# Performance work log

Measured on AMD Instinct MI355X. Metric: run time of the kernel, lower is better.

Reference implementation:

```python
import jax, jax.numpy as jnp
import numpy as np

D_MODEL = 768
N_HEADS = 12
D_K = 768
D_V = 768
SEQ = 2048
BATCH = 2


def setup_inputs() -> dict:
    key = jax.random.key(0)
    ks = jax.random.split(key, 9)
    s = 0.02
    return {
        "x": jax.random.normal(ks[0], (SEQ, BATCH, D_MODEL), dtype=jnp.float32),
        "Wq": jax.random.normal(ks[1], (D_MODEL, D_K), dtype=jnp.float32) * s,
        "bq": jnp.zeros((D_K,), dtype=jnp.float32),
        "Wk": jax.random.normal(ks[2], (D_MODEL, D_K), dtype=jnp.float32) * s,
        "bk": jnp.zeros((D_K,), dtype=jnp.float32),
        "Wv": jax.random.normal(ks[3], (D_MODEL, D_V), dtype=jnp.float32) * s,
        "bv": jnp.zeros((D_V,), dtype=jnp.float32),
        "Wo": jax.random.normal(ks[4], (D_V, D_MODEL), dtype=jnp.float32) * s,
        "bo": jnp.zeros((D_MODEL,), dtype=jnp.float32),
    }


def reference(x, Wq, bq, Wk, bk, Wv, bv, Wo, bo):
    # x: (S, B, D)
    S, B, D = x.shape
    H = N_HEADS
    hk = D_K // H
    hv = D_V // H
    q = (x @ Wq + bq).reshape(S, B, H, hk)
    k = (x @ Wk + bk).reshape(S, B, H, hk)
    v = (x @ Wv + bv).reshape(S, B, H, hv)
    scale = 1.0 / np.sqrt(hk).astype(np.float32)
    # scores: (B, H, S_q, S_k)
    att = jnp.einsum("sbhd,tbhd->bhst", q, k) * scale
    causal = jnp.triu(jnp.ones((S, S), dtype=bool), k=1)  # True above diagonal
    att = jnp.where(causal, jnp.float32(-jnp.inf), att)
    att = jax.nn.softmax(att, axis=-1)
    y = jnp.einsum("bhst,tbhd->sbhd", att, v).reshape(S, B, D_V)
    return y @ Wo + bo  # (S, B, D)
```

## Files before the change

### kernel.cpp

```cpp
#include <hip/hip_runtime.h>

typedef __attribute__((ext_vector_type(8))) short short8;
typedef __attribute__((ext_vector_type(4))) short s16x4;
typedef __attribute__((ext_vector_type(4))) float f32x4;

#define NHEADS 12
#define SEQLEN 2048
#define HEADD  64
#define DMODEL 768

__device__ __forceinline__ short cvtbf(float f) {
  unsigned u = __builtin_bit_cast(unsigned, f);
  u += 0x7fffu + ((u >> 16) & 1u);
  return (short)(u >> 16);
}

__device__ __forceinline__ void gload16(const void* g, void* l) {
  __builtin_amdgcn_global_load_lds((const __attribute__((address_space(1))) void*)g,
                                   (__attribute__((address_space(3))) void*)l, 16, 0, 0);
}

__device__ __forceinline__ void ds_write_hi16(short* p, float v) {
  asm volatile("ds_write_b16_d16_hi %0, %1"
               : : "v"((__attribute__((address_space(3))) short*)p), "v"(v) : "memory");
}

__global__ void prep_kernel(const float* __restrict__ x, short* __restrict__ xb,
                            const float* __restrict__ w0, const float* __restrict__ w1,
                            const float* __restrict__ w2, const float* __restrict__ w3,
                            short* __restrict__ wt, short* __restrict__ wot) {
  __shared__ float t[32][33];
  const int tid = threadIdx.x;
  if (blockIdx.x < 1536) {
    int i = blockIdx.x * 256 + tid;
    const float* p = x + (size_t)i * 8;
    short8 v;
#pragma unroll
    for (int j = 0; j < 8; ++j) v[j] = cvtbf(p[j]);
    *(short8*)(xb + (size_t)i * 8) = v;
    return;
  }
  int bx = blockIdx.x - 1536;
  int bz = bx / 576, rem = bx - bz * 576;
  int bxx = rem % 24, byy = rem / 24;
  const float* W = bz == 0 ? w0 : bz == 1 ? w1 : bz == 2 ? w2 : w3;
  short* O = bz < 3 ? wt + (size_t)bz * (768 * 768) : wot;
  int tx = tid & 31, ty = tid >> 5;
  int n0 = bxx * 32, k0 = byy * 32;
#pragma unroll
  for (int j = 0; j < 4; ++j)
    t[ty + j * 8][tx] = W[(k0 + ty + j * 8) * 768 + n0 + tx];
  __syncthreads();
#pragma unroll
  for (int j = 0; j < 4; ++j)
    O[(n0 + ty + j * 8) * 768 + k0 + tx] = cvtbf(t[tx][ty + j * 8]);
}

template <bool DBUF>
__device__ __forceinline__ void gemm_core128(const short* __restrict__ A,
                                             const short* __restrict__ Bt,
                                             short* sA, short* sB,
                                             int bm, int bn, f32x4 acc[4][4]) {
  const int tid = threadIdx.x;
  const int w = tid >> 6, lane = tid & 63;
  const int quad = lane >> 4, l16 = lane & 15;
  const int wm = (w & 1) * 64, wn = (w >> 1) * 64;

  int gA[4], gB[4], lbase[4];
#pragma unroll
  for (int j = 0; j < 4; ++j) {
    int slot = j * 256 + w * 64 + lane;
    int r = slot >> 3, c = (slot & 7) ^ (r & 7);
    gA[j] = (bm * 128 + r) * 768 + c * 8;
    gB[j] = (bn * 128 + r) * 768 + c * 8;
    lbase[j] = (j * 256 + w * 64) * 8;
  }

  if (DBUF) {
#pragma unroll
    for (int j = 0; j < 4; ++j) {
      gload16(A + gA[j], sA + lbase[j]);
      gload16(Bt + gB[j], sB + lbase[j]);
    }
    int pb = 0;
    for (int kt = 0; kt < 12; ++kt) {
      __syncthreads();
      if (kt + 1 < 12) {
        int o = (pb ^ 1) * 8192;
#pragma unroll
        for (int j = 0; j < 4; ++j) {
          gload16(A + gA[j] + (kt + 1) * 64, sA + o + lbase[j]);
          gload16(Bt + gB[j] + (kt + 1) * 64, sB + o + lbase[j]);
        }
      }
      const short* pa = sA + pb * 8192;
      const short* pbv = sB + pb * 8192;
#pragma unroll
      for (int ks = 0; ks < 2; ++ks) {
        int cp = (ks * 4 + quad) ^ (l16 & 7);
        short8 a[4], b[4];
#pragma unroll
        for (int mt = 0; mt < 4; ++mt)
          a[mt] = *(const short8*)(pa + (wm + mt * 16 + l16) * 64 + cp * 8);
#pragma unroll
        for (int nt = 0; nt < 4; ++nt)
          b[nt] = *(const short8*)(pbv + (wn + nt * 16 + l16) * 64 + cp * 8);
#pragma unroll
        for (int mt = 0; mt < 4; ++mt)
#pragma unroll
          for (int nt = 0; nt < 4; ++nt)
            acc[mt][nt] = __builtin_amdgcn_mfma_f32_16x16x32_bf16(a[mt], b[nt], acc[mt][nt], 0, 0, 0);
      }
      pb ^= 1;
    }
  } else {
    for (int kt = 0; kt < 12; ++kt) {
      __syncthreads();
#pragma unroll
      for (int j = 0; j < 4; ++j) {
        gload16(A + gA[j] + kt * 64, sA + lbase[j]);
        gload16(Bt + gB[j] + kt * 64, sB + lbase[j]);
      }
      __syncthreads();
#pragma unroll
      for (int ks = 0; ks < 2; ++ks) {
        int cp = (ks * 4 + quad) ^ (l16 & 7);
        short8 a[4], b[4];
#pragma unroll
        for (int mt = 0; mt < 4; ++mt)
          a[mt] = *(const short8*)(sA + (wm + mt * 16 + l16) * 64 + cp * 8);
#pragma unroll
        for (int nt = 0; nt < 4; ++nt)
          b[nt] = *(const short8*)(sB + (wn + nt * 16 + l16) * 64 + cp * 8);
#pragma unroll
        for (int mt = 0; mt < 4; ++mt)
#pragma unroll
          for (int nt = 0; nt < 4; ++nt)
            acc[mt][nt] = __builtin_amdgcn_mfma_f32_16x16x32_bf16(a[mt], b[nt], acc[mt][nt], 0, 0, 0);
      }
    }
  }
}

__global__ __launch_bounds__(256, 3) void qkv_gemm(
    const short* __restrict__ A, const short* __restrict__ Bt,
    const float* __restrict__ bq, const float* __restrict__ bk, const float* __restrict__ bv,
    short* __restrict__ oq, short* __restrict__ ok, short* __restrict__ ov) {
  __shared__ short sA[128 * 64];
  __shared__ short sB[128 * 64];
  f32x4 acc[4][4];
  const f32x4 z4 = {0.f, 0.f, 0.f, 0.f};
#pragma unroll
  for (int mt = 0; mt < 4; ++mt)
#pragma unroll
    for (int nt = 0; nt < 4; ++nt) acc[mt][nt] = z4;

  const int bm = blockIdx.x, bn = blockIdx.y;
  gemm_core128<false>(A, Bt, sA, sB, bm, bn, acc);

  const int seg = bn / 6, bn_l = bn % 6;
  const float* bias = seg == 0 ? bq : seg == 1 ? bk : bv;
  short* outp = seg == 0 ? oq : seg == 1 ? ok : ov;

  const int tid = threadIdx.x;
  const int w = tid >> 6, lane = tid & 63;
  const int quad = lane >> 4, l16 = lane & 15;
  const int wm = (w & 1) * 64, wn = (w >> 1) * 64;

#pragma unroll
  for (int nt = 0; nt < 4; ++nt) {
    int n = bn_l * 128 + wn + nt * 16 + l16;
    float bval = bias[n];
    int h = n >> 6, d = n & 63;
#pragma unroll
    for (int mt = 0; mt < 4; ++mt) {
      int rowb = wm + mt * 16 + quad * 4;
#pragma unroll
      for (int r = 0; r < 4; ++r) {
        int m = bm * 128 + rowb + r;
        int s = m >> 1, b = m & 1;
        float v = acc[mt][nt][r] + bval;
        if (seg == 0) v *= 0.1803368801f;
        if (seg < 2)
          outp[((b * NHEADS + h) * SEQLEN + s) * HEADD + d] = cvtbf(v);
        else
          outp[((b * NHEADS + h) * HEADD + d) * SEQLEN + s] = cvtbf(v);
      }
    }
  }
}

#define AE(qi, ts, nt) ((qi) | ((ts) << 8) | ((nt) << 16))
__device__ const int ATTN_TAB[80] = {
  AE(31,0,8), AE(31,8,8), AE(31,16,8), AE(31,24,8),
  AE(30,0,8), AE(30,8,8), AE(30,16,8),
  AE(29,0,8), AE(29,8,8), AE(29,16,8),
  AE(28,0,8), AE(28,8,8), AE(28,16,8),
  AE(27,0,8), AE(27,8,8), AE(27,16,8),
  AE(26,0,8), AE(26,8,8), AE(26,16,8),
  AE(25,0,8), AE(25,8,8), AE(25,16,8),
  AE(24,0,8), AE(24,8,8), AE(24,16,8),
  AE(23,0,8), AE(23,8,8), AE(23,16,8),
  AE(22,0,8), AE(22,8,8),
  AE(21,0,8), AE(21,8,8),
  AE(20,0,8), AE(20,8,8),
  AE(19,0,8), AE(19,8,8),
  AE(18,0,8), AE(18,8,8),
  AE(17,0,8), AE(17,8,8),
  AE(16,0,8), AE(16,8,8),
  AE(15,0,8), AE(15,8,8),
  AE(14,0,8), AE(13,0,8), AE(12,0,8), AE(11,0,8),
  AE(10,0,8), AE(9,0,8),  AE(8,0,8),  AE(7,0,8),
  AE(30,24,7), AE(22,16,7), AE(14,8,7), AE(6,0,7),
  AE(29,24,6), AE(21,16,6), AE(13,8,6), AE(5,0,6),
  AE(28,24,5), AE(20,16,5), AE(12,8,5), AE(4,0,5),
  AE(27,24,4), AE(19,16,4), AE(11,8,4), AE(3,0,4),
  AE(26,24,3), AE(18,16,3), AE(10,8,3), AE(2,0,3),
  AE(25,24,2), AE(17,16,2), AE(9,8,2),  AE(1,0,2),
  AE(24,24,1), AE(16,16,1), AE(8,8,1),  AE(0,0,1),
};
__device__ const int PBASE[32] = {
  0,0,0,0,0,0,0,0,
  0,2,4,6,8,10,12,14,
  16,19,22,25,28,31,34,37,
  40,44,48,52,56,60,64,68};

__global__ __launch_bounds__(128, 2) void attn_kernel(
    const short* __restrict__ Q, const short* __restrict__ K,
    const short* __restrict__ Vt, short* __restrict__ Y,
    float* __restrict__ Of, float* __restrict__ lf) {
  __shared__ short sK[2][64 * 64];
  __shared__ short sV[2][64 * 64];
  __shared__ short sP[64 * 64];
  const int tid = threadIdx.x;
  const int w = tid >> 6, lane = tid & 63;
  const int quad = lane >> 4, l16 = lane & 15;
  const int e = ATTN_TAB[blockIdx.x / 24];
  const int bh = blockIdx.x % 24;
  const int qi = e & 255, ts = (e >> 8) & 255, ntl = e >> 16;
  const int q0 = qi << 6;
  const short* Qb = Q + (size_t)bh * (SEQLEN * HEADD);
  const short* Kb = K + (size_t)bh * (SEQLEN * HEADD);
  const short* Vb = Vt + (size_t)bh * (SEQLEN * HEADD);

  short8 aq[2][2];
#pragma unroll
  for (int m = 0; m < 2; ++m)
#pragma unroll
    for (int ks = 0; ks < 2; ++ks)
      aq[m][ks] = *(const short8*)(Qb + (q0 + w * 32 + m * 16 + l16) * 64 + ks * 32 + quad * 8);

  const short8 bones = {0x3F80, 0x3F80, 0x3F80, 0x3F80, 0x3F80, 0x3F80, 0x3F80, 0x3F80};
  f32x4 acc_o[2][4], acc_l[2];
  const f32x4 z4 = {0.f, 0.f, 0.f, 0.f};
#pragma unroll
  for (int m = 0; m < 2; ++m) {
#pragma unroll
    for (int nt = 0; nt < 4; ++nt) acc_o[m][nt] = z4;
    acc_l[m] = z4;
  }

  int gK[4], gV[4], lbase[4];
#pragma unroll
  for (int j = 0; j < 4; ++j) {
    int slot = j * 128 + w * 64 + lane;
    int r = slot >> 3, c = (slot & 7) ^ (r & 7);
    gK[j] = r * 64 + c * 8;
    gV[j] = r * 2048 + c * 8;
    lbase[j] = (j * 128 + w * 64) * 8;
  }

  const int tend = ts + ntl;

#pragma unroll
  for (int j = 0; j < 4; ++j) {
    gload16(Kb + (ts << 6) * 64 + gK[j], &sK[0][lbase[j]]);
    gload16(Vb + (ts << 6) + gV[j], &sV[0][lbase[j]]);
  }

  int pb = 0;
  for (int it = ts; it < tend; ++it) {
    __syncthreads();
    if (it + 1 < tend) {
      const int t1 = (it + 1) << 6;
#pragma unroll
      for (int j = 0; j < 4; ++j) {
        gload16(Kb + t1 * 64 + gK[j], &sK[pb ^ 1][lbase[j]]);
        gload16(Vb + t1 + gV[j], &sV[pb ^ 1][lbase[j]]);
      }
    }
    const short* sk = sK[pb];
    const short* sv = sV[pb];

    f32x4 sc[2][4];
#pragma unroll
    for (int m = 0; m < 2; ++m)
#pragma unroll
      for (int nt = 0; nt < 4; ++nt) sc[m][nt] = z4;
    __builtin_amdgcn_s_setprio(1);
#pragma unroll
    for (int ks = 0; ks < 2; ++ks) {
      int cp = (ks * 4 + quad) ^ (l16 & 7);
#pragma unroll
      for (int nt = 0; nt < 4; ++nt) {
        short8 bk = *(const short8*)(sk + (nt * 16 + l16) * 64 + cp * 8);
#pragma unroll
        for (int m = 0; m < 2; ++m)
          sc[m][nt] = __builtin_amdgcn_mfma_f32_16x16x32_bf16(aq[m][ks], bk, sc[m][nt], 0, 0, 0);
      }
    }
    __builtin_amdgcn_s_setprio(0);

    if (it == qi) {
      const int t0 = it << 6;
#pragma unroll
      for (int m = 0; m < 2; ++m) {
        int qrow = q0 + w * 32 + m * 16 + quad * 4;
#pragma unroll
        for (int nt = 0; nt < 4; ++nt)
#pragma unroll
          for (int r = 0; r < 4; ++r) {
            int t = t0 + nt * 16 + l16;
            if (t > qrow + r) sc[m][nt][r] = -1e30f;
          }
      }
    }

#pragma unroll
    for (int m = 0; m < 2; ++m)
#pragma unroll
      for (int nt = 0; nt < 4; ++nt)
#pragma unroll
        for (int r = 0; r < 4; ++r) {
          float p = __builtin_amdgcn_exp2f(sc[m][nt][r]);
          int rq = w * 32 + m * 16 + quad * 4 + r;
          int t = nt * 16 + l16;
          int c = t >> 3;
          ds_write_hi16(&sP[rq * 64 + ((c ^ (rq & 7)) * 8 + (t & 7))], p);
        }

    __builtin_amdgcn_s_setprio(1);
#pragma unroll
    for (int kst = 0; kst < 2; ++kst) {
      short8 ap[2];
#pragma unroll
      for (int m = 0; m < 2; ++m) {
        int rq = w * 32 + m * 16 + l16;
        int cpa = (kst * 4 + quad) ^ (rq & 7);
        ap[m] = *(const short8*)(sP + rq * 64 + cpa * 8);
        acc_l[m] = __builtin_amdgcn_mfma_f32_16x16x32_bf16(ap[m], bones, acc_l[m], 0, 0, 0);
      }
#pragma unroll
      for (int nt = 0; nt < 4; ++nt) {
        int row = nt * 16 + l16;
        int cv = (kst * 4 + quad) ^ (row & 7);
        short8 bv = *(const short8*)(sv + row * 64 + cv * 8);
#pragma unroll
        for (int m = 0; m < 2; ++m)
          acc_o[m][nt] = __builtin_amdgcn_mfma_f32_16x16x32_bf16(ap[m], bv, acc_o[m][nt], 0, 0, 0);
      }
    }
    __builtin_amdgcn_s_setprio(0);
    pb ^= 1;
  }

  if (qi < 8) {
    const int b = bh / NHEADS, h = bh % NHEADS;
#pragma unroll
    for (int m = 0; m < 2; ++m)
#pragma unroll
      for (int r = 0; r < 4; ++r) {
        float rl = __builtin_amdgcn_rcpf(acc_l[m][r]);
        int srow = q0 + w * 32 + m * 16 + quad * 4 + r;
#pragma unroll
        for (int nt = 0; nt < 4; ++nt)
          Y[(srow * 2 + b) * DMODEL + h * 64 + nt * 16 + l16] = cvtbf(acc_o[m][nt][r] * rl);
      }
  } else {
    const int slot = bh * 72 + PBASE[qi] + (ts >> 3);
    float* Ob = Of + (size_t)slot * 4096;
#pragma unroll
    for (int m = 0; m < 2; ++m)
#pragma unroll
      for (int r = 0; r < 4; ++r) {
        int row = w * 32 + m * 16 + quad * 4 + r;
#pragma unroll
        for (int nt = 0; nt < 4; ++nt)
          Ob[row * 64 + nt * 16 + l16] = acc_o[m][nt][r];
        if (l16 == 0) lf[slot * 64 + row] = acc_l[m][r];
      }
  }
}

__global__ void attn_merge(const float* __restrict__ Of, const float* __restrict__ lf,
                           short* __restrict__ Y) {
  const int bh = blockIdx.x % 24, qi = 8 + blockIdx.x / 24;
  const int nch = (qi >> 3) + 1;
  const int base = bh * 72 + PBASE[qi];
  const float* O0 = Of + (size_t)base * 4096;
  const float* L0 = lf + base * 64;
  const int b = bh / NHEADS, h = bh % NHEADS;
  const int tid = threadIdx.x;
#pragma unroll
  for (int j = 0; j < 4; ++j) {
    int i4 = j * 256 + tid;
    int row = i4 >> 4, col4 = (i4 & 15) * 4;
    f32x4 o = *(const f32x4*)(O0 + (size_t)i4 * 4);
    float l = L0[row];
    for (int c = 1; c < nch; ++c) {
      o += *(const f32x4*)(O0 + (size_t)c * 4096 + (size_t)i4 * 4);
      l += L0[c * 64 + row];
    }
    float rl = __builtin_amdgcn_rcpf(l);
    s16x4 y;
#pragma unroll
    for (int k = 0; k < 4; ++k) y[k] = cvtbf(o[k] * rl);
    int srow = qi * 64 + row;
    *(s16x4*)(Y + (size_t)(srow * 2 + b) * DMODEL + h * 64 + col4) = y;
  }
}

__global__ __launch_bounds__(256, 2) void oproj_gemm(
    const short* __restrict__ A, const short* __restrict__ Bt,
    const float* __restrict__ bo, float* __restrict__ out) {
  __shared__ short sA[2 * 128 * 64];
  __shared__ short sB[2 * 128 * 64];
  f32x4 acc[4][4];
  const f32x4 z4 = {0.f, 0.f, 0.f, 0.f};
#pragma unroll
  for (int mt = 0; mt < 4; ++mt)
#pragma unroll
    for (int nt = 0; nt < 4; ++nt) acc[mt][nt] = z4;

  const int bm = blockIdx.x, bn = blockIdx.y;
  gemm_core128<true>(A, Bt, sA, sB, bm, bn, acc);

  const int tid = threadIdx.x;
  const int w = tid >> 6, lane = tid & 63;
  const int quad = lane >> 4, l16 = lane & 15;
  const int wm = (w & 1) * 64, wn = (w >> 1) * 64;

#pragma unroll
  for (int nt = 0; nt < 4; ++nt) {
    int n = bn * 128 + wn + nt * 16 + l16;
    float bval = bo[n];
#pragma unroll
    for (int mt = 0; mt < 4; ++mt) {
      int rowb = wm + mt * 16 + quad * 4;
#pragma unroll
      for (int r = 0; r < 4; ++r) {
        int m = bm * 128 + rowb + r;
        out[(size_t)m * 768 + n] = acc[mt][nt][r] + bval;
      }
    }
  }
}

extern "C" void kernel_launch(void* const* d_in, const int* in_sizes, int n_in,
                              void* d_out, int out_size, void* d_ws, size_t ws_size,
                              hipStream_t stream) {
  const float* x  = (const float*)d_in[0];
  const float* Wq = (const float*)d_in[1];
  const float* bq = (const float*)d_in[2];
  const float* Wk = (const float*)d_in[3];
  const float* bk = (const float*)d_in[4];
  const float* Wv = (const float*)d_in[5];
  const float* bv = (const float*)d_in[6];
  const float* Wo = (const float*)d_in[7];
  const float* bo = (const float*)d_in[8];
  float* out = (float*)d_out;

  short* ws  = (short*)d_ws;
  short* xb  = ws;
  short* wt  = ws + 3145728;
  short* wot = ws + 4915200;
  short* qw  = ws + 5505024;
  short* kw  = ws + 8650752;
  short* vw  = ws + 11796480;
  short* yw  = ws + 14942208;
  float* Of  = (float*)(ws + 18087936);
  float* lf  = Of + 7077888;

  prep_kernel<<<3840, 256, 0, stream>>>(x, xb, Wq, Wk, Wv, Wo, wt, wot);
  qkv_gemm<<<dim3(32, 18), 256, 0, stream>>>(xb, wt, bq, bk, bv, qw, kw, vw);
  attn_kernel<<<1920, 128, 0, stream>>>(qw, kw, vw, yw, Of, lf);
  attn_merge<<<576, 256, 0, stream>>>(Of, lf, yw);
  oproj_gemm<<<dim3(32, 6), 256, 0, stream>>>(yw, wot, bo, out);
}
```

Before: 157.2 us.

## Double attention query tile to 128 rows per block with new split-K schedule

The attention kernel now processes 128 query rows per block with 4 waves (256 threads), so each staged K/V tile is shared by twice as many queries. The work table is rebuilt for 16 query pairs with uneven KV chunk splits, the partial-output buffers and merge kernel are resized to 128-row slots, and the causal mask now applies for any tile at or past the diagonal pair. The s_setprio hints are removed. This cuts the number of blocks and redundant K/V loads, but it raises LDS and register pressure per block and changes load balance.

```diff
diff --git a/kernel.cpp b/kernel.cpp
--- a/kernel.cpp
+++ b/kernel.cpp
@@ -190,55 +190,47 @@
   }
 }
 
-#define AE(qi, ts, nt) ((qi) | ((ts) << 8) | ((nt) << 16))
-__device__ const int ATTN_TAB[80] = {
-  AE(31,0,8), AE(31,8,8), AE(31,16,8), AE(31,24,8),
-  AE(30,0,8), AE(30,8,8), AE(30,16,8),
-  AE(29,0,8), AE(29,8,8), AE(29,16,8),
-  AE(28,0,8), AE(28,8,8), AE(28,16,8),
-  AE(27,0,8), AE(27,8,8), AE(27,16,8),
-  AE(26,0,8), AE(26,8,8), AE(26,16,8),
-  AE(25,0,8), AE(25,8,8), AE(25,16,8),
-  AE(24,0,8), AE(24,8,8), AE(24,16,8),
-  AE(23,0,8), AE(23,8,8), AE(23,16,8),
-  AE(22,0,8), AE(22,8,8),
-  AE(21,0,8), AE(21,8,8),
-  AE(20,0,8), AE(20,8,8),
-  AE(19,0,8), AE(19,8,8),
-  AE(18,0,8), AE(18,8,8),
-  AE(17,0,8), AE(17,8,8),
-  AE(16,0,8), AE(16,8,8),
-  AE(15,0,8), AE(15,8,8),
-  AE(14,0,8), AE(13,0,8), AE(12,0,8), AE(11,0,8),
-  AE(10,0,8), AE(9,0,8),  AE(8,0,8),  AE(7,0,8),
-  AE(30,24,7), AE(22,16,7), AE(14,8,7), AE(6,0,7),
-  AE(29,24,6), AE(21,16,6), AE(13,8,6), AE(5,0,6),
-  AE(28,24,5), AE(20,16,5), AE(12,8,5), AE(4,0,5),
-  AE(27,24,4), AE(19,16,4), AE(11,8,4), AE(3,0,4),
-  AE(26,24,3), AE(18,16,3), AE(10,8,3), AE(2,0,3),
-  AE(25,24,2), AE(17,16,2), AE(9,8,2),  AE(1,0,2),
-  AE(24,24,1), AE(16,16,1), AE(8,8,1),  AE(0,0,1),
+#define AE(qip, ts, nt, ci) ((qip) | ((ts) << 8) | ((nt) << 16) | ((ci) << 24))
+__device__ const int ATTN_TAB[40] = {
+  AE(15,0,8,0), AE(15,8,8,1), AE(15,16,8,2), AE(15,24,8,3),
+  AE(14,0,8,0), AE(14,8,8,1),
+  AE(11,0,8,0), AE(11,8,8,1), AE(11,16,8,2),
+  AE(10,0,8,0),
+  AE(7,0,8,0),  AE(7,8,8,1),
+  AE(3,0,8,0),
+  AE(14,16,7,2), AE(14,23,7,3),
+  AE(13,0,7,0), AE(13,7,7,1), AE(13,14,7,2), AE(13,21,7,3),
+  AE(12,0,7,0), AE(12,7,7,1),
+  AE(10,8,7,1), AE(10,15,7,2),
+  AE(9,0,7,0),  AE(9,7,7,1),
+  AE(6,0,7,0),  AE(6,7,7,1),
+  AE(12,14,6,2), AE(12,20,6,3),
+  AE(9,14,6,2),
+  AE(8,0,6,0),  AE(8,6,6,1), AE(8,12,6,2),
+  AE(5,0,6,0),  AE(5,6,6,1),
+  AE(2,0,6,0),
+  AE(4,0,5,0),  AE(4,5,5,1),
+  AE(1,0,4,0),
+  AE(0,0,2,0),
 };
-__device__ const int PBASE[32] = {
-  0,0,0,0,0,0,0,0,
-  0,2,4,6,8,10,12,14,
-  16,19,22,25,28,31,34,37,
-  40,44,48,52,56,60,64,68};
-
-__global__ __launch_bounds__(128, 2) void attn_kernel(
+__device__ const int PBASE[16] = {
+  0,0,0,0, 0,2,4,6, 8,11,14,17, 20,24,28,32};
+
+__global__ __launch_bounds__(256, 3) void attn_kernel(
     const short* __restrict__ Q, const short* __restrict__ K,
     const short* __restrict__ Vt, short* __restrict__ Y,
     float* __restrict__ Of, float* __restrict__ lf) {
   __shared__ short sK[2][64 * 64];
   __shared__ short sV[2][64 * 64];
-  __shared__ short sP[64 * 64];
+  __shared__ short sP[128 * 64];
   const int tid = threadIdx.x;
   const int w = tid >> 6, lane = tid & 63;
   const int quad = lane >> 4, l16 = lane & 15;
   const int e = ATTN_TAB[blockIdx.x / 24];
   const int bh = blockIdx.x % 24;
-  const int qi = e & 255, ts = (e >> 8) & 255, ntl = e >> 16;
-  const int q0 = qi << 6;
+  const int qip = e & 255, ts = (e >> 8) & 255, ntl = (e >> 16) & 255, ci = e >> 24;
+  const int q0 = qip << 7;
+  const int qi2 = qip << 1;
   const short* Qb = Q + (size_t)bh * (SEQLEN * HEADD);
   const short* Kb = K + (size_t)bh * (SEQLEN * HEADD);
   const short* Vb = Vt + (size_t)bh * (SEQLEN * HEADD);
@@ -260,20 +252,20 @@
     acc_l[m] = z4;
   }
 
-  int gK[4], gV[4], lbase[4];
-#pragma unroll
-  for (int j = 0; j < 4; ++j) {
-    int slot = j * 128 + w * 64 + lane;
+  int gK[2], gV[2], lbase[2];
+#pragma unroll
+  for (int j = 0; j < 2; ++j) {
+    int slot = j * 256 + w * 64 + lane;
     int r = slot >> 3, c = (slot & 7) ^ (r & 7);
     gK[j] = r * 64 + c * 8;
     gV[j] = r * 2048 + c * 8;
-    lbase[j] = (j * 128 + w * 64) * 8;
+    lbase[j] = (j * 256 + w * 64) * 8;
   }
 
   const int tend = ts + ntl;
 
 #pragma unroll
-  for (int j = 0; j < 4; ++j) {
+  for (int j = 0; j < 2; ++j) {
     gload16(Kb + (ts << 6) * 64 + gK[j], &sK[0][lbase[j]]);
     gload16(Vb + (ts << 6) + gV[j], &sV[0][lbase[j]]);
   }
@@ -284,7 +276,7 @@
     if (it + 1 < tend) {
       const int t1 = (it + 1) << 6;
 #pragma unroll
-      for (int j = 0; j < 4; ++j) {
+      for (int j = 0; j < 2; ++j) {
         gload16(Kb + t1 * 64 + gK[j], &sK[pb ^ 1][lbase[j]]);
         gload16(Vb + t1 + gV[j], &sV[pb ^ 1][lbase[j]]);
       }
@@ -297,7 +289,6 @@
     for (int m = 0; m < 2; ++m)
 #pragma unroll
       for (int nt = 0; nt < 4; ++nt) sc[m][nt] = z4;
-    __builtin_amdgcn_s_setprio(1);
 #pragma unroll
     for (int ks = 0; ks < 2; ++ks) {
       int cp = (ks * 4 + quad) ^ (l16 & 7);
@@ -309,9 +300,8 @@
           sc[m][nt] = __builtin_amdgcn_mfma_f32_16x16x32_bf16(aq[m][ks], bk, sc[m][nt], 0, 0, 0);
       }
     }
-    __builtin_amdgcn_s_setprio(0);
-
-    if (it == qi) {
+
+    if (it >= qi2) {
       const int t0 = it << 6;
 #pragma unroll
       for (int m = 0; m < 2; ++m) {
@@ -339,7 +329,6 @@
           ds_write_hi16(&sP[rq * 64 + ((c ^ (rq & 7)) * 8 + (t & 7))], p);
         }
 
-    __builtin_amdgcn_s_setprio(1);
 #pragma unroll
     for (int kst = 0; kst < 2; ++kst) {
       short8 ap[2];
@@ -360,11 +349,10 @@
           acc_o[m][nt] = __builtin_amdgcn_mfma_f32_16x16x32_bf16(ap[m], bv, acc_o[m][nt], 0, 0, 0);
       }
     }
-    __builtin_amdgcn_s_setprio(0);
     pb ^= 1;
   }
 
-  if (qi < 8) {
+  if (qip < 4) {
     const int b = bh / NHEADS, h = bh % NHEADS;
 #pragma unroll
     for (int m = 0; m < 2; ++m)
@@ -377,8 +365,8 @@
           Y[(srow * 2 + b) * DMODEL + h * 64 + nt * 16 + l16] = cvtbf(acc_o[m][nt][r] * rl);
       }
   } else {
-    const int slot = bh * 72 + PBASE[qi] + (ts >> 3);
-    float* Ob = Of + (size_t)slot * 4096;
+    const int slot = bh * 36 + PBASE[qip] + ci;
+    float* Ob = Of + (size_t)slot * 8192;
 #pragma unroll
     for (int m = 0; m < 2; ++m)
 #pragma unroll
@@ -387,35 +375,35 @@
 #pragma unroll
         for (int nt = 0; nt < 4; ++nt)
           Ob[row * 64 + nt * 16 + l16] = acc_o[m][nt][r];
-        if (l16 == 0) lf[slot * 64 + row] = acc_l[m][r];
+        if (l16 == 0) lf[slot * 128 + row] = acc_l[m][r];
       }
   }
 }
 
 __global__ void attn_merge(const float* __restrict__ Of, const float* __restrict__ lf,
                            short* __restrict__ Y) {
-  const int bh = blockIdx.x % 24, qi = 8 + blockIdx.x / 24;
-  const int nch = (qi >> 3) + 1;
-  const int base = bh * 72 + PBASE[qi];
-  const float* O0 = Of + (size_t)base * 4096;
-  const float* L0 = lf + base * 64;
+  const int bh = blockIdx.x % 24, qip = 4 + blockIdx.x / 24;
+  const int nch = qip < 8 ? 2 : qip < 12 ? 3 : 4;
+  const int base = bh * 36 + PBASE[qip];
+  const float* O0 = Of + (size_t)base * 8192;
+  const float* L0 = lf + base * 128;
   const int b = bh / NHEADS, h = bh % NHEADS;
   const int tid = threadIdx.x;
 #pragma unroll
-  for (int j = 0; j < 4; ++j) {
+  for (int j = 0; j < 8; ++j) {
     int i4 = j * 256 + tid;
     int row = i4 >> 4, col4 = (i4 & 15) * 4;
     f32x4 o = *(const f32x4*)(O0 + (size_t)i4 * 4);
     float l = L0[row];
     for (int c = 1; c < nch; ++c) {
-      o += *(const f32x4*)(O0 + (size_t)c * 4096 + (size_t)i4 * 4);
-      l += L0[c * 64 + row];
+      o += *(const f32x4*)(O0 + (size_t)c * 8192 + (size_t)i4 * 4);
+      l += L0[c * 128 + row];
     }
     float rl = __builtin_amdgcn_rcpf(l);
     s16x4 y;
 #pragma unroll
     for (int k = 0; k < 4; ++k) y[k] = cvtbf(o[k] * rl);
-    int srow = qi * 64 + row;
+    int srow = qip * 128 + row;
     *(s16x4*)(Y + (size_t)(srow * 2 + b) * DMODEL + h * 64 + col4) = y;
   }
 }
@@ -483,7 +471,7 @@
 
   prep_kernel<<<3840, 256, 0, stream>>>(x, xb, Wq, Wk, Wv, Wo, wt, wot);
   qkv_gemm<<<dim3(32, 18), 256, 0, stream>>>(xb, wt, bq, bk, bv, qw, kw, vw);
-  attn_kernel<<<1920, 128, 0, stream>>>(qw, kw, vw, yw, Of, lf);
-  attn_merge<<<576, 256, 0, stream>>>(Of, lf, yw);
+  attn_kernel<<<960, 256, 0, stream>>>(qw, kw, vw, yw, Of, lf);
+  attn_merge<<<288, 256, 0, stream>>>(Of, lf, yw);
   oproj_gemm<<<dim3(32, 6), 256, 0, stream>>>(yw, wot, bo, out);
 }
```

Result: no change. 159.9 us (+1.7%).
